# Performance work log

Hardware: AMD Instinct MI355X
Metric: run time of the kernel (lower is better)

The kernel has to match this reference:

```python
import jax, jax.numpy as jnp
import numpy as np
import math

B, L, HID = 2, 2048, 1024
NH, DH = 16, 64
MASK_VAL = -1000000000.0  # half_precision_flag == False


def setup_inputs() -> dict:
    key = jax.random.key(0)
    ks = jax.random.split(key, 12)
    s = 0.02
    return {
        "queries": jax.random.normal(ks[0], (B, L, HID), jnp.float32),
        "keys": jax.random.normal(ks[1], (B, L, HID), jnp.float32),
        "values": jax.random.normal(ks[2], (B, L, HID), jnp.float32),
        "mask": jax.random.randint(ks[3], (B, L, L), 0, 2, jnp.int32),
        "Wq": jax.random.normal(ks[4], (HID, NH * DH), jnp.float32) * s,
        "bq": jnp.zeros((NH * DH,), jnp.float32),
        "Wk": jax.random.normal(ks[5], (HID, NH * DH), jnp.float32) * s,
        "bk": jnp.zeros((NH * DH,), jnp.float32),
        "Wv": jax.random.normal(ks[6], (HID, NH * DH), jnp.float32) * s,
        "bv": jnp.zeros((NH * DH,), jnp.float32),
        "Wo": jax.random.normal(ks[7], (NH * DH, HID), jnp.float32) * s,
        "bo": jnp.zeros((HID,), jnp.float32),
    }


def reference(queries, keys, values, mask, Wq, bq, Wk, bk, Wv, bv, Wo, bo):
    # Linear projections: (B, L, NH*DH)
    q = queries @ Wq + bq
    k = keys @ Wk + bk
    v = values @ Wv + bv
    # FAITHFUL to original: raw .view(B, NH, -1, DH) without transpose
    q = q.reshape(B, NH, L, DH)
    k = k.reshape(B, NH, L, DH)
    v = v.reshape(B, NH, L, DH)
    # scaled dot-product scores: (B, NH, L, L)
    scores = jnp.einsum("bhqd,bhkd->bhqk", q, k) / math.sqrt(DH)
    scores = jnp.where(mask[:, None, :, :] == 0, MASK_VAL, scores)
    probs = jax.nn.softmax(scores, axis=-1)  # dropout p=0 -> identity
    ctx = jnp.einsum("bhqk,bhkd->bhqd", probs, v)  # (B, NH, L, DH)
    # transpose(1,2) then flatten heads, as in original
    ctx = ctx.transpose(0, 2, 1, 3).reshape(B, L, NH * DH)
    return ctx @ Wo + bo
```

## Files before the change

kernel.cpp:

```cpp
#include <hip/hip_runtime.h>
#include <stdint.h>

typedef __bf16 bf16;
typedef __bf16 bf16x8 __attribute__((ext_vector_type(8)));
typedef __bf16 bf16x4 __attribute__((ext_vector_type(4)));
typedef float  f32x4  __attribute__((ext_vector_type(4)));
typedef short  s16x4  __attribute__((ext_vector_type(4)));
typedef unsigned long long ull;

#define GLOAD16(gptr, lptr)                                                     \
  __builtin_amdgcn_global_load_lds(                                             \
      (const __attribute__((address_space(1))) void*)(gptr),                    \
      (__attribute__((address_space(3))) void*)(lptr), 16, 0, 0)

#define MFMA16(a, b, c) __builtin_amdgcn_mfma_f32_16x16x32_bf16((a), (b), (c), 0, 0, 0)
#define MFMA16K16(a, b, c) __builtin_amdgcn_mfma_f32_16x16x16bf16_1k((a), (b), (c), 0, 0, 0)

static constexpr int B_ = 2, L_ = 2048, NH_ = 16, DH_ = 64;
static constexpr float QSCALE = 0.18033688011112042f;

__global__ __launch_bounds__(256) void k_prep(const float* __restrict__ q,
                                              const float* __restrict__ k,
                                              const float* __restrict__ v,
                                              const int* __restrict__ mask,
                                              const float* __restrict__ wq,
                                              const float* __restrict__ wk,
                                              const float* __restrict__ wv,
                                              const float* __restrict__ wo,
                                              bf16* __restrict__ X,
                                              bf16* __restrict__ Wt,
                                              ull* __restrict__ mb) {
  __shared__ float t[32][33];
  const int bid = blockIdx.x, tid = threadIdx.x;
  if (bid < 32768) {
    int tt = bid * 256 + tid;
    ull bal = __ballot(mask[tt] != 0);
    if ((tid & 63) == 0) mb[tt >> 6] = bal;
  } else if (bid < 45056) {
    int u = bid - 32768;
    int z = u >> 12, x = u & 4095;
    const float* in = z == 0 ? q : (z == 1 ? k : v);
    bf16* out = X + (size_t)z * 4194304;
    int i = x * 256 + tid;
    const float4 f = ((const float4*)in)[i];
    bf16x4 o = {(bf16)f.x, (bf16)f.y, (bf16)f.z, (bf16)f.w};
    ((bf16x4*)out)[i] = o;
  } else {
    int u = bid - 45056;
    int z = u >> 10, rem = u & 1023;
    const float* in = z == 0 ? wq : (z == 1 ? wk : (z == 2 ? wv : wo));
    bf16* out = Wt + (size_t)z * 1048576;
    int bx = (rem & 31) * 32, by = (rem >> 5) * 32;
    int x = tid & 31, y = tid >> 5;
#pragma unroll
    for (int r = 0; r < 4; ++r)
      t[y + r * 8][x] = in[(size_t)(by + y + r * 8) * 1024 + bx + x];
    __syncthreads();
#pragma unroll
    for (int r = 0; r < 4; ++r)
      out[(size_t)(bx + y + r * 8) * 1024 + by + x] = (bf16)t[x][y + r * 8];
  }
}

__global__ __launch_bounds__(256) void k_gemm3(const bf16* __restrict__ Xb,
                                               const bf16* __restrict__ Wb,
                                               const float* __restrict__ b0,
                                               const float* __restrict__ b1,
                                               const float* __restrict__ b2,
                                               bf16* __restrict__ Ob) {
  const int z = blockIdx.z;
  const bf16* A  = Xb + (size_t)z * 4194304;
  const bf16* Bt = Wb + (size_t)z * 1048576;
  const float* bias = z == 0 ? b0 : (z == 1 ? b1 : b2);
  bf16* C = Ob + (size_t)z * 4194304;
  const int m0 = blockIdx.y * 128, n0 = blockIdx.x * 128;
  __shared__ __align__(16) bf16 As[128 * 32];
  __shared__ __align__(16) bf16 Bs[128 * 32];
  const int tid = threadIdx.x, lane = tid & 63, w = tid >> 6, quad = lane >> 4, l15 = lane & 15;
  const int wm = (w & 1) * 64, wn = (w >> 1) * 64;
  f32x4 acc[4][4] = {};
  for (int kt = 0; kt < 32; ++kt) {
    const int kk = kt * 32;
#pragma unroll
    for (int i = 0; i < 2; ++i) {
      int s = tid + i * 256;
      int r = s >> 2, c = (s & 3) ^ ((r >> 1) & 3);
      GLOAD16(A + (size_t)(m0 + r) * 1024 + kk + c * 8, As + s * 8);
      GLOAD16(Bt + (size_t)(n0 + r) * 1024 + kk + c * 8, Bs + s * 8);
    }
    __syncthreads();
    bf16x8 af[4], bb[4];
#pragma unroll
    for (int i = 0; i < 4; ++i) {
      int ra = wm + i * 16 + l15, rb = wn + i * 16 + l15;
      af[i] = *(const bf16x8*)(As + (ra * 4 + (quad ^ ((ra >> 1) & 3))) * 8);
      bb[i] = *(const bf16x8*)(Bs + (rb * 4 + (quad ^ ((rb >> 1) & 3))) * 8);
    }
#pragma unroll
    for (int mi = 0; mi < 4; ++mi)
#pragma unroll
      for (int ni = 0; ni < 4; ++ni)
        acc[mi][ni] = MFMA16(af[mi], bb[ni], acc[mi][ni]);
    __syncthreads();
  }
  const float scale = (z == 0) ? QSCALE : 1.0f;
#pragma unroll
  for (int mi = 0; mi < 4; ++mi)
#pragma unroll
    for (int ni = 0; ni < 4; ++ni) {
      int row = m0 + wm + mi * 16 + quad * 4;
      int col = n0 + wn + ni * 16 + l15;
      float bz = bias[col];
      if (z == 2) {
        int b_ = row >> 11, l = row & 2047;
        int hh = l >> 7;
        int i0 = (l & 127) * 16 + (col >> 6);
        int d  = col & 63;
        bf16* dst = C + (size_t)(b_ * 16 + hh) * 131072;
#pragma unroll
        for (int r = 0; r < 4; ++r) {
          int iK = i0 + 16 * r;
          dst[((size_t)(iK >> 2) * 64 + d) * 4 + (iK & 3)] = (bf16)(acc[mi][ni][r] + bz);
        }
      } else {
#pragma unroll
        for (int r = 0; r < 4; ++r)
          C[(size_t)(row + r) * 1024 + col] = (bf16)((acc[mi][ni][r] + bz) * scale);
      }
    }
}

__global__ __launch_bounds__(256) void k_gemmo(const bf16* __restrict__ A,
                                               const bf16* __restrict__ Bt,
                                               const float* __restrict__ bias,
                                               float* __restrict__ C) {
  const int m0 = blockIdx.y * 64, n0 = blockIdx.x * 128;
  __shared__ __align__(16) bf16 As[64 * 32];
  __shared__ __align__(16) bf16 Bs[128 * 32];
  const int tid = threadIdx.x, lane = tid & 63, w = tid >> 6, quad = lane >> 4, l15 = lane & 15;
  const int wn = w * 32;
  f32x4 acc[4][2] = {};
  for (int kt = 0; kt < 32; ++kt) {
    const int kk = kt * 32;
    {
      int r = tid >> 2, c = (tid & 3) ^ ((r >> 1) & 3);
      GLOAD16(A + (size_t)(m0 + r) * 1024 + kk + c * 8, As + tid * 8);
    }
#pragma unroll
    for (int i = 0; i < 2; ++i) {
      int s = tid + i * 256;
      int r = s >> 2, c = (s & 3) ^ ((r >> 1) & 3);
      GLOAD16(Bt + (size_t)(n0 + r) * 1024 + kk + c * 8, Bs + s * 8);
    }
    __syncthreads();
    bf16x8 af[4], bb[2];
#pragma unroll
    for (int i = 0; i < 4; ++i) {
      int ra = i * 16 + l15;
      af[i] = *(const bf16x8*)(As + (ra * 4 + (quad ^ ((ra >> 1) & 3))) * 8);
    }
#pragma unroll
    for (int i = 0; i < 2; ++i) {
      int rb = wn + i * 16 + l15;
      bb[i] = *(const bf16x8*)(Bs + (rb * 4 + (quad ^ ((rb >> 1) & 3))) * 8);
    }
#pragma unroll
    for (int mi = 0; mi < 4; ++mi)
#pragma unroll
      for (int ni = 0; ni < 2; ++ni)
        acc[mi][ni] = MFMA16(af[mi], bb[ni], acc[mi][ni]);
    __syncthreads();
  }
#pragma unroll
  for (int mi = 0; mi < 4; ++mi)
#pragma unroll
    for (int ni = 0; ni < 2; ++ni) {
      int row = m0 + mi * 16 + quad * 4;
      int col = n0 + wn + ni * 16 + l15;
      float bz = bias[col];
#pragma unroll
      for (int r = 0; r < 4; ++r)
        C[(size_t)(row + r) * 1024 + col] = acc[mi][ni][r] + bz;
    }
}

__global__ __launch_bounds__(256) void k_flash(const bf16* __restrict__ Qp,
                                               const bf16* __restrict__ Kp,
                                               const bf16* __restrict__ Vtp,
                                               const ull* __restrict__ mb,
                                               bf16* __restrict__ ctx) {
  const int b = blockIdx.z, h = blockIdx.y, q0 = blockIdx.x * 128;
  const size_t HEAD = 131072;
  const bf16* Q  = Qp  + ((size_t)b * NH_ + h) * HEAD;
  const bf16* K  = Kp  + ((size_t)b * NH_ + h) * HEAD;
  const bf16* Vt = Vtp + ((size_t)b * NH_ + h) * HEAD;
  const ull* mrow = mb + (size_t)b * L_ * 32;

  __shared__ __align__(16) bf16 Ks[2][64 * 64];
  __shared__ __align__(16) bf16 Vs[2][64 * 64];
  __shared__ __align__(16) ull  Ms[2][256];

  const int tid = threadIdx.x, lane = tid & 63, w = tid >> 6, quad = lane >> 4, l15 = lane & 15;

  bf16x8 qf[2][2];
#pragma unroll
  for (int qb = 0; qb < 2; ++qb)
#pragma unroll
    for (int ks = 0; ks < 2; ++ks)
      qf[qb][ks] = *(const bf16x8*)(Q + (size_t)(q0 + w * 32 + qb * 16 + l15) * 64 + ks * 32 + quad * 8);

#pragma unroll
  for (int i = 0; i < 2; ++i) {
    int s = tid + i * 256;
    int key = s >> 3, c = (s & 7) ^ (key & 7);
    GLOAD16(K + (size_t)key * 64 + c * 8, Ks[0] + s * 8);
    GLOAD16(Vt + (size_t)s * 8, Vs[0] + s * 8);
  }
  if (w < 2) {
    int r = w * 64 + lane;
    GLOAD16(mrow + (size_t)(q0 + r) * 32, (bf16*)&Ms[0][0] + r * 8);
  }
  __syncthreads();

  f32x4 accO[2][4] = {};
  f32x4 accL[2] = {};
  const s16x4 onesf = {0x3F80, 0x3F80, 0x3F80, 0x3F80};

  for (int kt = 0; kt < 32; ++kt) {
    const int cur = kt & 1;
    if (kt + 1 < 32) {
      const int nxt = cur ^ 1;
#pragma unroll
      for (int i = 0; i < 2; ++i) {
        int s = tid + i * 256;
        int key = s >> 3, c = (s & 7) ^ (key & 7);
        GLOAD16(K + (size_t)((kt + 1) * 64 + key) * 64 + c * 8, Ks[nxt] + s * 8);
        GLOAD16(Vt + (size_t)(kt + 1) * 4096 + s * 8, Vs[nxt] + s * 8);
      }
      if ((kt & 1) && w < 2) {
        int r = w * 64 + lane;
        GLOAD16(mrow + (size_t)(q0 + r) * 32 + (kt + 1),
                (bf16*)&Ms[((kt + 1) >> 1) & 1][0] + r * 8);
      }
    }

    f32x4 st[4][2] = {};
#pragma unroll
    for (int ks = 0; ks < 2; ++ks)
#pragma unroll
      for (int kb = 0; kb < 4; ++kb) {
        int key = kb * 16 + l15;
        bf16x8 kf = *(const bf16x8*)(Ks[cur] + (key * 8 + ((ks * 4 + quad) ^ (key & 7))) * 8);
        st[kb][0] = MFMA16(kf, qf[0][ks], st[kb][0]);
        st[kb][1] = MFMA16(kf, qf[1][ks], st[kb][1]);
      }

    const ull* Mcur = Ms[(kt >> 1) & 1];
    const ull word0 = Mcur[(w * 32 + l15) * 2 + cur];
    const ull word1 = Mcur[(w * 32 + 16 + l15) * 2 + cur];
    s16x4 pf[4][2];
#pragma unroll
    for (int kb = 0; kb < 4; ++kb)
#pragma unroll
      for (int qb = 0; qb < 2; ++qb) {
        const unsigned nib = (unsigned)((qb ? word1 : word0) >> (kb * 16 + quad * 4)) & 0xFu;
        float p0 = (nib & 1u) ? __builtin_amdgcn_exp2f(st[kb][qb][0]) : 0.f;
        float p1 = (nib & 2u) ? __builtin_amdgcn_exp2f(st[kb][qb][1]) : 0.f;
        float p2 = (nib & 4u) ? __builtin_amdgcn_exp2f(st[kb][qb][2]) : 0.f;
        float p3 = (nib & 8u) ? __builtin_amdgcn_exp2f(st[kb][qb][3]) : 0.f;
        bf16x4 pb = {(bf16)p0, (bf16)p1, (bf16)p2, (bf16)p3};
        pf[kb][qb] = __builtin_bit_cast(s16x4, pb);
      }

#pragma unroll
    for (int kb = 0; kb < 4; ++kb) {
      accL[0] = MFMA16K16(pf[kb][0], onesf, accL[0]);
      accL[1] = MFMA16K16(pf[kb][1], onesf, accL[1]);
    }

#pragma unroll
    for (int kb = 0; kb < 4; ++kb)
#pragma unroll
      for (int db = 0; db < 4; ++db) {
        s16x4 vf = *(const s16x4*)(Vs[cur] + ((size_t)((kb * 4 + quad) * 64 + db * 16 + l15)) * 4);
        accO[0][db] = MFMA16K16(pf[kb][0], vf, accO[0][db]);
        accO[1][db] = MFMA16K16(pf[kb][1], vf, accO[1][db]);
      }
    __syncthreads();
  }

#pragma unroll
  for (int qb = 0; qb < 2; ++qb) {
    float rl[4];
#pragma unroll
    for (int r = 0; r < 4; ++r) rl[r] = 1.0f / accL[qb][r];
#pragma unroll
    for (int db = 0; db < 4; ++db) {
      const int col = h * 64 + db * 16 + l15;
#pragma unroll
      for (int r = 0; r < 4; ++r) {
        const int rowg = q0 + w * 32 + qb * 16 + quad * 4 + r;
        ctx[((size_t)b * L_ + rowg) * 1024 + col] = (bf16)(accO[qb][db][r] * rl[r]);
      }
    }
  }
}

extern "C" void kernel_launch(void* const* d_in, const int* in_sizes, int n_in,
                              void* d_out, int out_size, void* d_ws, size_t ws_size,
                              hipStream_t stream) {
  (void)in_sizes; (void)n_in; (void)out_size; (void)ws_size;
  const float* q    = (const float*)d_in[0];
  const float* k    = (const float*)d_in[1];
  const float* v    = (const float*)d_in[2];
  const int*   mask = (const int*)d_in[3];
  const float* Wq = (const float*)d_in[4];
  const float* bq = (const float*)d_in[5];
  const float* Wk = (const float*)d_in[6];
  const float* bk = (const float*)d_in[7];
  const float* Wv = (const float*)d_in[8];
  const float* bv = (const float*)d_in[9];
  const float* Wo = (const float*)d_in[10];
  const float* bo = (const float*)d_in[11];
  float* out = (float*)d_out;

  char* ws = (char*)d_ws;
  const size_t SX = (size_t)4096 * 1024 * 2;
  const size_t SW = (size_t)1024 * 1024 * 2;
  bf16* X   = (bf16*)(ws);
  bf16* Wt  = (bf16*)(ws + 3 * SX);
  bf16* QKV = (bf16*)(ws + 3 * SX + 4 * SW);
  bf16* Qp  = QKV;
  bf16* Kp  = QKV + 4194304;
  bf16* Vtp = QKV + 2 * 4194304;
  bf16* Ctx = (bf16*)(ws + 6 * SX + 4 * SW);
  ull* mbits = (ull*)(ws + 7 * SX + 4 * SW);

  dim3 blk(256);
  k_prep<<<49152, blk, 0, stream>>>(q, k, v, mask, Wq, Wk, Wv, Wo, X, Wt, mbits);

  k_gemm3<<<dim3(8, 32, 3), blk, 0, stream>>>(X, Wt, bq, bk, bv, QKV);

  k_flash<<<dim3(16, NH_, B_), blk, 0, stream>>>(Qp, Kp, Vtp, mbits, Ctx);

  k_gemmo<<<dim3(8, 64), blk, 0, stream>>>(Ctx, Wt + 3 * 1048576, bo, out);
}
```

Measured before the change: 275.4 us.

## Split flash attention block into 8 waves of 16 query rows each

The flash-attention kernel now runs 512 threads per block instead of 256. Each of the 8 waves handles 16 query rows rather than 32, and each thread issues one K/V tile load instead of two. The aim is more waves in flight and fewer live accumulators per thread, to hide memory and exp latency better. In exchange, every K and V fragment read from LDS feeds only one query block instead of two, which doubles LDS read traffic per MFMA and adds block-wide synchronisation across more waves.

Result: faster. 268.2 us (-2.6%).

```diff
diff --git a/kernel.cpp b/kernel.cpp
--- a/kernel.cpp
+++ b/kernel.cpp
@@ -184,7 +184,7 @@
     }
 }
 
-__global__ __launch_bounds__(256) void k_flash(const bf16* __restrict__ Qp,
+__global__ __launch_bounds__(512) void k_flash(const bf16* __restrict__ Qp,
                                                const bf16* __restrict__ Kp,
                                                const bf16* __restrict__ Vtp,
                                                const ull* __restrict__ mb,
@@ -202,16 +202,13 @@
 
   const int tid = threadIdx.x, lane = tid & 63, w = tid >> 6, quad = lane >> 4, l15 = lane & 15;
 
-  bf16x8 qf[2][2];
-#pragma unroll
-  for (int qb = 0; qb < 2; ++qb)
-#pragma unroll
-    for (int ks = 0; ks < 2; ++ks)
-      qf[qb][ks] = *(const bf16x8*)(Q + (size_t)(q0 + w * 32 + qb * 16 + l15) * 64 + ks * 32 + quad * 8);
-
-#pragma unroll
-  for (int i = 0; i < 2; ++i) {
-    int s = tid + i * 256;
+  bf16x8 qf[2];
+#pragma unroll
+  for (int ks = 0; ks < 2; ++ks)
+    qf[ks] = *(const bf16x8*)(Q + (size_t)(q0 + w * 16 + l15) * 64 + ks * 32 + quad * 8);
+
+  {
+    int s = tid;
     int key = s >> 3, c = (s & 7) ^ (key & 7);
     GLOAD16(K + (size_t)key * 64 + c * 8, Ks[0] + s * 8);
     GLOAD16(Vt + (size_t)s * 8, Vs[0] + s * 8);
@@ -222,21 +219,18 @@
   }
   __syncthreads();
 
-  f32x4 accO[2][4] = {};
-  f32x4 accL[2] = {};
+  f32x4 accO[4] = {};
+  f32x4 accL = {};
   const s16x4 onesf = {0x3F80, 0x3F80, 0x3F80, 0x3F80};
 
   for (int kt = 0; kt < 32; ++kt) {
     const int cur = kt & 1;
     if (kt + 1 < 32) {
       const int nxt = cur ^ 1;
-#pragma unroll
-      for (int i = 0; i < 2; ++i) {
-        int s = tid + i * 256;
-        int key = s >> 3, c = (s & 7) ^ (key & 7);
-        GLOAD16(K + (size_t)((kt + 1) * 64 + key) * 64 + c * 8, Ks[nxt] + s * 8);
-        GLOAD16(Vt + (size_t)(kt + 1) * 4096 + s * 8, Vs[nxt] + s * 8);
-      }
+      int s = tid;
+      int key = s >> 3, c = (s & 7) ^ (key & 7);
+      GLOAD16(K + (size_t)((kt + 1) * 64 + key) * 64 + c * 8, Ks[nxt] + s * 8);
+      GLOAD16(Vt + (size_t)(kt + 1) * 4096 + s * 8, Vs[nxt] + s * 8);
       if ((kt & 1) && w < 2) {
         int r = w * 64 + lane;
         GLOAD16(mrow + (size_t)(q0 + r) * 32 + (kt + 1),
@@ -244,64 +238,54 @@
       }
     }
 
-    f32x4 st[4][2] = {};
+    f32x4 st[4] = {};
 #pragma unroll
     for (int ks = 0; ks < 2; ++ks)
 #pragma unroll
       for (int kb = 0; kb < 4; ++kb) {
         int key = kb * 16 + l15;
         bf16x8 kf = *(const bf16x8*)(Ks[cur] + (key * 8 + ((ks * 4 + quad) ^ (key & 7))) * 8);
-        st[kb][0] = MFMA16(kf, qf[0][ks], st[kb][0]);
-        st[kb][1] = MFMA16(kf, qf[1][ks], st[kb][1]);
+        st[kb] = MFMA16(kf, qf[ks], st[kb]);
       }
 
     const ull* Mcur = Ms[(kt >> 1) & 1];
-    const ull word0 = Mcur[(w * 32 + l15) * 2 + cur];
-    const ull word1 = Mcur[(w * 32 + 16 + l15) * 2 + cur];
-    s16x4 pf[4][2];
+    const ull word = Mcur[(w * 16 + l15) * 2 + cur];
+    s16x4 pf[4];
+#pragma unroll
+    for (int kb = 0; kb < 4; ++kb) {
+      const unsigned nib = (unsigned)(word >> (kb * 16 + quad * 4)) & 0xFu;
+      float p0 = (nib & 1u) ? __builtin_amdgcn_exp2f(st[kb][0]) : 0.f;
+      float p1 = (nib & 2u) ? __builtin_amdgcn_exp2f(st[kb][1]) : 0.f;
+      float p2 = (nib & 4u) ? __builtin_amdgcn_exp2f(st[kb][2]) : 0.f;
+      float p3 = (nib & 8u) ? __builtin_amdgcn_exp2f(st[kb][3]) : 0.f;
+      bf16x4 pb = {(bf16)p0, (bf16)p1, (bf16)p2, (bf16)p3};
+      pf[kb] = __builtin_bit_cast(s16x4, pb);
+    }
+
 #pragma unroll
     for (int kb = 0; kb < 4; ++kb)
-#pragma unroll
-      for (int qb = 0; qb < 2; ++qb) {
-        const unsigned nib = (unsigned)((qb ? word1 : word0) >> (kb * 16 + quad * 4)) & 0xFu;
-        float p0 = (nib & 1u) ? __builtin_amdgcn_exp2f(st[kb][qb][0]) : 0.f;
-        float p1 = (nib & 2u) ? __builtin_amdgcn_exp2f(st[kb][qb][1]) : 0.f;
-        float p2 = (nib & 4u) ? __builtin_amdgcn_exp2f(st[kb][qb][2]) : 0.f;
-        float p3 = (nib & 8u) ? __builtin_amdgcn_exp2f(st[kb][qb][3]) : 0.f;
-        bf16x4 pb = {(bf16)p0, (bf16)p1, (bf16)p2, (bf16)p3};
-        pf[kb][qb] = __builtin_bit_cast(s16x4, pb);
-      }
-
-#pragma unroll
-    for (int kb = 0; kb < 4; ++kb) {
-      accL[0] = MFMA16K16(pf[kb][0], onesf, accL[0]);
-      accL[1] = MFMA16K16(pf[kb][1], onesf, accL[1]);
-    }
+      accL = MFMA16K16(pf[kb], onesf, accL);
 
 #pragma unroll
     for (int kb = 0; kb < 4; ++kb)
 #pragma unroll
       for (int db = 0; db < 4; ++db) {
         s16x4 vf = *(const s16x4*)(Vs[cur] + ((size_t)((kb * 4 + quad) * 64 + db * 16 + l15)) * 4);
-        accO[0][db] = MFMA16K16(pf[kb][0], vf, accO[0][db]);
-        accO[1][db] = MFMA16K16(pf[kb][1], vf, accO[1][db]);
+        accO[db] = MFMA16K16(pf[kb], vf, accO[db]);
       }
     __syncthreads();
   }
 
-#pragma unroll
-  for (int qb = 0; qb < 2; ++qb) {
-    float rl[4];
-#pragma unroll
-    for (int r = 0; r < 4; ++r) rl[r] = 1.0f / accL[qb][r];
-#pragma unroll
-    for (int db = 0; db < 4; ++db) {
-      const int col = h * 64 + db * 16 + l15;
-#pragma unroll
-      for (int r = 0; r < 4; ++r) {
-        const int rowg = q0 + w * 32 + qb * 16 + quad * 4 + r;
-        ctx[((size_t)b * L_ + rowg) * 1024 + col] = (bf16)(accO[qb][db][r] * rl[r]);
-      }
+  float rl[4];
+#pragma unroll
+  for (int r = 0; r < 4; ++r) rl[r] = 1.0f / accL[r];
+#pragma unroll
+  for (int db = 0; db < 4; ++db) {
+    const int col = h * 64 + db * 16 + l15;
+#pragma unroll
+    for (int r = 0; r < 4; ++r) {
+      const int rowg = q0 + w * 16 + quad * 4 + r;
+      ctx[((size_t)b * L_ + rowg) * 1024 + col] = (bf16)(accO[db][r] * rl[r]);
     }
   }
 }
@@ -341,7 +325,7 @@
 
   k_gemm3<<<dim3(8, 32, 3), blk, 0, stream>>>(X, Wt, bq, bk, bv, QKV);
 
-  k_flash<<<dim3(16, NH_, B_), blk, 0, stream>>>(Qp, Kp, Vtp, mbits, Ctx);
+  k_flash<<<dim3(16, NH_, B_), dim3(512), 0, stream>>>(Qp, Kp, Vtp, mbits, Ctx);
 
   k_gemmo<<<dim3(8, 64), blk, 0, stream>>>(Ctx, Wt + 3 * 1048576, bo, out);
 }
```
